# Kernel optimization log

Hardware: AMD Instinct MI355X
Metric: run time of the kernel (lower is better)

Reference implementation:

```python
import jax, jax.numpy as jnp
import numpy as np
from jax import lax

B, L = 8, 128
V, P = 30000, 50
EMB, POS = 300, 30
H = 256            # rnn_hidden per direction
H2 = 2 * H         # BiLSTM output dim
NBIO, NLAB = 9, 10
ROUNDS = 2
IN = EMB + POS
NEG = -100000000000.0


def setup_inputs() -> dict:
    key = jax.random.key(0)
    ks = jax.random.split(key, 25)
    tokens = jax.random.randint(ks[0], (B, L), 1, V)
    pos = jax.random.randint(ks[1], (B, L), 1, P)
    lens = jax.random.randint(ks[2], (B,), L // 2, L + 1)
    mask_s = (jnp.arange(L)[None, :] < lens[:, None]).astype(jnp.float32)

    def g(k, shape, s=0.05):
        return jax.random.normal(k, shape, dtype=jnp.float32) * s

    return dict(
        tokens=tokens, pos=pos, mask_s=mask_s,
        emb=g(ks[3], (V, EMB), 0.5), pos_emb=g(ks[4], (P, POS), 0.5),
        Wih_f=g(ks[5], (4 * H, IN)), Whh_f=g(ks[6], (4 * H, H)), b_f=g(ks[7], (4 * H,)),
        Wih_b=g(ks[8], (4 * H, IN)), Whh_b=g(ks[9], (4 * H, H)), b_b=g(ks[10], (4 * H,)),
        Wg_ih=g(ks[11], (3 * H2, NBIO)), Wg_hh=g(ks[12], (3 * H2, H2)),
        bg_ih=g(ks[13], (3 * H2,)), bg_hh=g(ks[14], (3 * H2,)),
        Wr_ih=g(ks[15], (3 * H2, NLAB)), Wr_hh=g(ks[16], (3 * H2, H2)),
        br_ih=g(ks[17], (3 * H2,)), br_hh=g(ks[18], (3 * H2,)),
        W_Lr=g(ks[19], (H2, 2 * H2)), b_Lr=g(ks[20], (H2,)),
        W_Cr=g(ks[21], (NLAB, H2)), b_Cr=g(ks[22], (NLAB,)),
        W_Cg=g(ks[23], (NBIO, H2)), b_Cg=g(ks[24], (NBIO,)),
    )


def lstm_dir(x, m, Wih, Whh, b, reverse):
    # x: [B,L,IN], m: [B,L]. Masked updates emulate pack_padded_sequence
    # (state held at padded steps; padded outputs zeroed by caller).
    Bn = x.shape[0]
    h0 = jnp.zeros((Bn, H), x.dtype)
    c0 = jnp.zeros((Bn, H), x.dtype)

    def step(carry, inp):
        h, c = carry
        xt, mt = inp  # [B,IN], [B,1]
        gates = xt @ Wih.T + h @ Whh.T + b
        i, f, g, o = jnp.split(gates, 4, axis=-1)
        i = jax.nn.sigmoid(i); f = jax.nn.sigmoid(f)
        g = jnp.tanh(g); o = jax.nn.sigmoid(o)
        c_new = f * c + i * g
        h_new = o * jnp.tanh(c_new)
        h = mt * h_new + (1.0 - mt) * h
        c = mt * c_new + (1.0 - mt) * c
        return (h, c), h

    xs = (jnp.swapaxes(x, 0, 1), m.T[:, :, None])
    _, hs = lax.scan(step, (h0, c0), xs, reverse=reverse)
    return jnp.swapaxes(hs, 0, 1)  # [B,L,H]


def gru_cell(x, h, Wih, Whh, bih, bhh):
    gi = x @ Wih.T + bih
    gh = h @ Whh.T + bhh
    ir, iz, inn = jnp.split(gi, 3, axis=-1)
    hr, hz, hn = jnp.split(gh, 3, axis=-1)
    r = jax.nn.sigmoid(ir + hr)
    z = jax.nn.sigmoid(iz + hz)
    n = jnp.tanh(inn + r * hn)
    return (1.0 - z) * n + z * h


def pair_scores(Hr, W_Lr, b_Lr, W_Cr, b_Cr):
    # Lr([e1;e2]) split: e12 @ W_Lr.T = e1 @ W1.T + e2 @ W2.T (avoids 4H concat)
    W1, W2 = W_Lr[:, :H2], W_Lr[:, H2:]
    a = jnp.einsum('blh,oh->blo', Hr, W1)  # [B,L,H2]
    b2 = jnp.einsum('blh,oh->blo', Hr, W2)
    e = jax.nn.relu(a[:, :, None, :] + b2[:, None, :, :] + b_Lr)  # [B,L,L,H2]
    return jax.nn.sigmoid(jnp.einsum('bsth,kh->bstk', e, W_Cr) + b_Cr)  # [B,L,L,NLAB]


def reference(tokens, pos, mask_s, emb, pos_emb,
              Wih_f, Whh_f, b_f, Wih_b, Whh_b, b_b,
              Wg_ih, Wg_hh, bg_ih, bg_hh,
              Wr_ih, Wr_hh, br_ih, br_hh,
              W_Lr, b_Lr, W_Cr, b_Cr, W_Cg, b_Cg):
    x = jnp.concatenate([emb[tokens], pos_emb[pos]], axis=2)  # [B,L,IN]
    hf = lstm_dir(x, mask_s, Wih_f, Whh_f, b_f, reverse=False)
    hb = lstm_dir(x, mask_s, Wih_b, Whh_b, b_b, reverse=True)
    Henc = jnp.concatenate([hf, hb], axis=2) * mask_s[:, :, None]  # [B,L,H2]

    m2 = mask_s[:, :, None] * mask_s[:, None, :]  # [B,L,L] pair mask
    m3 = m2[:, :, :, None]                        # [B,L,L,1]

    Hc, Hg, Hr = Henc, Henc, Henc
    for _ in range(ROUNDS):
        prob_Cg = jax.nn.softmax(Hg @ W_Cg.T + b_Cg, axis=2)        # [B,L,NBIO]
        prob_Cr = pair_scores(Hr, W_Lr, b_Lr, W_Cr, b_Cr)            # [B,L,L,NLAB]
        prob_Cr = jnp.where(m3 > 0, prob_Cr, NEG)
        prob_Cr = prob_Cr.max(axis=2)                                # [B,L,NLAB]
        hflat = Hc.reshape(-1, H2)
        Hg = gru_cell(prob_Cg.reshape(-1, NBIO), hflat, Wg_ih, Wg_hh, bg_ih, bg_hh).reshape(Hc.shape)
        Hr = gru_cell(prob_Cr.reshape(-1, NLAB), hflat, Wr_ih, Wr_hh, br_ih, br_hh).reshape(Hc.shape)
        Hc = Hc + Hr + Hg

    logits_Cg = jax.nn.log_softmax(Hg @ W_Cg.T + b_Cg, axis=2) * mask_s[:, :, None]
    logits_Cr = pair_scores(Hr, W_Lr, b_Lr, W_Cr, b_Cr) * m3
    return logits_Cg, logits_Cr
```

## Files before the change

### kernel.cpp

```cpp
#include <hip/hip_runtime.h>
#include <hip/hip_bf16.h>
#include <stdint.h>

#define DEVI __device__ __forceinline__

static constexpr int Bn = 8, Ln = 128;
static constexpr int EMBc = 300, POSc = 30, INc = 330;
static constexpr int KPAD = 384;
static constexpr int Hc = 256, H2c = 512, G4 = 1024, G3 = 1536;
static constexpr int G2 = 2048;
static constexpr int GHW = 3072;
static constexpr int NBIOc = 9, NLABc = 10;
static constexpr float NEGc = -100000000000.0f;

typedef __attribute__((ext_vector_type(8))) short bf16x8;
typedef __attribute__((ext_vector_type(4))) float f32x4;

DEVI float sigf(float x) { return 1.0f / (1.0f + __expf(-x)); }

DEVI unsigned short b16rne(float f) {
    union { float f; unsigned u; } v; v.f = f;
    unsigned u = v.u;
    return (unsigned short)((u + 0x7FFFu + ((u >> 16) & 1u)) >> 16);
}

__global__ void k_prep0(const int* __restrict__ tok, const int* __restrict__ pos,
                        const float* __restrict__ emb, const float* __restrict__ pemb,
                        const float* __restrict__ WihF, const float* __restrict__ WihB,
                        const float* __restrict__ bF, const float* __restrict__ bB,
                        ushort* __restrict__ x, ushort* __restrict__ WihFB,
                        float* __restrict__ biasFB) {
    int i = blockIdx.x * 256 + threadIdx.x;
    const int N0 = Bn * Ln * KPAD;
    const int N1 = N0 + G2 * KPAD;
    if (i < N0) {
        int bl = i / KPAD, c = i - bl * KPAD;
        float v = 0.f;
        if (c < EMBc) v = emb[tok[bl] * EMBc + c];
        else if (c < INc) v = pemb[pos[bl] * POSc + (c - EMBc)];
        x[i] = b16rne(v);
    } else if (i < N1) {
        int w = i - N0;
        int r = w / KPAD, c = w - r * KPAD;
        float v = 0.f;
        if (c < INc) v = (r < G4) ? WihF[(size_t)r * INc + c] : WihB[(size_t)(r - G4) * INc + c];
        WihFB[w] = b16rne(v);
    } else if (i < N1 + G2) {
        int j = i - N1;
        biasFB[j] = (j < G4) ? bF[j] : bB[j - G4];
    }
}

__global__ __launch_bounds__(256) void k_gemm_bf(
    const ushort* __restrict__ A, const ushort* __restrict__ B,
    const float* __restrict__ bias, float* __restrict__ C, int M, int N, int K) {
    __shared__ __align__(16) ushort As[64][72];
    __shared__ __align__(16) ushort Bs[64][72];
    int tid = threadIdx.x;
    int lane = tid & 63, wv = tid >> 6;
    int m0 = blockIdx.y * 64, n0 = blockIdx.x * 64;
    int mw = (wv >> 1) * 32, nw = (wv & 1) * 32;
    int lr16 = lane & 15, g4 = lane >> 4;
    f32x4 acc[2][2] = {};
    for (int k0 = 0; k0 < K; k0 += 64) {
#pragma unroll
        for (int it = 0; it < 2; it++) {
            int idx = tid + it * 256;
            int r = idx >> 3, ch = idx & 7;
            uint4 av = *(const uint4*)(A + (size_t)(m0 + r) * K + k0 + ch * 8);
            *(uint4*)(&As[r][ch * 8]) = av;
            uint4 bv2 = *(const uint4*)(B + (size_t)(n0 + r) * K + k0 + ch * 8);
            *(uint4*)(&Bs[r][ch * 8]) = bv2;
        }
        __syncthreads();
#pragma unroll
        for (int ks = 0; ks < 2; ks++) {
            bf16x8 af[2], bfr[2];
#pragma unroll
            for (int i = 0; i < 2; i++) {
                af[i]  = *(const bf16x8*)(&As[mw + i * 16 + lr16][ks * 32 + g4 * 8]);
                bfr[i] = *(const bf16x8*)(&Bs[nw + i * 16 + lr16][ks * 32 + g4 * 8]);
            }
#pragma unroll
            for (int i = 0; i < 2; i++)
#pragma unroll
                for (int j = 0; j < 2; j++)
                    acc[i][j] = __builtin_amdgcn_mfma_f32_16x16x32_bf16(af[i], bfr[j], acc[i][j], 0, 0, 0);
        }
        __syncthreads();
    }
#pragma unroll
    for (int i = 0; i < 2; i++)
#pragma unroll
        for (int j = 0; j < 2; j++)
#pragma unroll
            for (int r2 = 0; r2 < 4; r2++) {
                int mm = m0 + mw + i * 16 + g4 * 4 + r2;
                int nn = n0 + nw + j * 16 + lr16;
                C[(size_t)mm * N + nn] = acc[i][j][r2] + (bias ? bias[nn] : 0.f);
            }
}

__global__ __launch_bounds__(512) void k_lstm_mfma(
    const float* __restrict__ Xpre,
    const float* __restrict__ WhhF, const float* __restrict__ WhhB,
    const float* __restrict__ mask, float* __restrict__ Henc,
    ushort* __restrict__ HencB, unsigned long long* __restrict__ hG,
    const float* __restrict__ Wg_hh, const float* __restrict__ Wr_hh,
    const float* __restrict__ W_Lr, const float* __restrict__ bg_hh,
    const float* __restrict__ br_hh,
    ushort* __restrict__ WhhGR, ushort* __restrict__ WLrAB, float* __restrict__ biasGR) {
    const int blk = blockIdx.x;
    const int tid = threadIdx.x;

    if (blk >= 8) {
        const int stride = 32 * 512;
        int pid = (blk - 8) * 512 + tid;
        for (int idx = pid; idx < GHW * H2c; idx += stride) {
            int r = idx >> 9, c = idx & 511;
            float v = (r < G3) ? Wg_hh[(size_t)r * H2c + c] : Wr_hh[(size_t)(r - G3) * H2c + c];
            WhhGR[idx] = b16rne(v);
        }
        for (int idx = pid; idx < G4 * H2c; idx += stride) {
            int r = idx >> 9, c = idx & 511;
            float v = (r < H2c) ? W_Lr[(size_t)r * (2 * H2c) + c]
                                : W_Lr[(size_t)(r - H2c) * (2 * H2c) + H2c + c];
            WLrAB[idx] = b16rne(v);
        }
        for (int idx = pid; idx < GHW; idx += stride)
            biasGR[idx] = (idx < G3) ? bg_hh[idx] : br_hh[idx - G3];
        return;
    }

    const int d = blk >> 2, q = blk & 3;
    const float* Whh = d ? WhhB : WhhF;
    const int lane = tid & 63, wv = tid >> 6;
    const int lr16 = lane & 15, g4 = lane >> 4;

    __shared__ __align__(16) uint32_t hlds[2][8 * 136];
    __shared__ float Glds[256][9];

    bf16x8 aw[16];
#pragma unroll
    for (int jt2 = 0; jt2 < 2; jt2++) {
        int jt = wv * 2 + jt2;
        int lr = jt * 16 + lr16;
        int g = lr >> 6, jj = lr & 63;
        int R = g * 256 + q * 64 + jj;
        const float* wr = Whh + (size_t)R * 256;
#pragma unroll
        for (int kt = 0; kt < 8; kt++) {
            int k0 = kt * 32 + g4 * 8;
            float4 f0 = *(const float4*)(wr + k0);
            float4 f1 = *(const float4*)(wr + k0 + 4);
            bf16x8 a;
            a[0] = (short)b16rne(f0.x); a[1] = (short)b16rne(f0.y);
            a[2] = (short)b16rne(f0.z); a[3] = (short)b16rne(f0.w);
            a[4] = (short)b16rne(f1.x); a[5] = (short)b16rne(f1.y);
            a[6] = (short)b16rne(f1.z); a[7] = (short)b16rne(f1.w);
            aw[jt2 * 8 + kt] = a;
        }
    }

    const int jj_t = tid & 63, b_t = tid >> 6;
    float hval = 0.f, cval = 0.f;
    const int bcol = lane & 15;
    const int bb = lane & 7;
    const int u1 = tid + 512;

    for (int s = 0; s < Ln; s++) {
        const int t = d ? (Ln - 1 - s) : s;

        const float* xrow = Xpre + ((size_t)(b_t * Ln + t)) * G2 + d * G4 + q * 64 + jj_t;
        float xg0 = xrow[0], xg1 = xrow[256], xg2 = xrow[512], xg3 = xrow[768];
        float mval = mask[b_t * Ln + t];

        const unsigned long long* slot = hG + ((size_t)(s & 1) * 2 + d) * 1024;
        unsigned long long ea, eb;
        do {
            ea = __hip_atomic_load(slot + tid, __ATOMIC_RELAXED, __HIP_MEMORY_SCOPE_AGENT);
            eb = __hip_atomic_load(slot + u1,  __ATOMIC_RELAXED, __HIP_MEMORY_SCOPE_AGENT);
        } while ((unsigned)(ea >> 32) != (unsigned)s || (unsigned)(eb >> 32) != (unsigned)s);
        uint32_t* hb = hlds[s & 1];
        hb[(tid >> 7) * 136 + (tid & 127)] = (uint32_t)ea;
        hb[(u1 >> 7) * 136 + (u1 & 127)]  = (uint32_t)eb;
        __syncthreads();

        bf16x8 bv[8];
#pragma unroll
        for (int kt = 0; kt < 8; kt++)
            bv[kt] = *(const bf16x8*)(&hb[bb * 136 + kt * 16 + g4 * 4]);

        f32x4 acc0 = {0.f, 0.f, 0.f, 0.f}, acc1 = {0.f, 0.f, 0.f, 0.f};
#pragma unroll
        for (int kt = 0; kt < 8; kt++) {
            acc0 = __builtin_amdgcn_mfma_f32_16x16x32_bf16(aw[kt], bv[kt], acc0, 0, 0, 0);
            acc1 = __builtin_amdgcn_mfma_f32_16x16x32_bf16(aw[8 + kt], bv[kt], acc1, 0, 0, 0);
        }

        if (bcol < 8) {
            int lrb0 = (wv * 2 + 0) * 16 + g4 * 4;
            int lrb1 = (wv * 2 + 1) * 16 + g4 * 4;
#pragma unroll
            for (int r2 = 0; r2 < 4; r2++) Glds[lrb0 + r2][bcol] = acc0[r2];
#pragma unroll
            for (int r2 = 0; r2 < 4; r2++) Glds[lrb1 + r2][bcol] = acc1[r2];
        }
        __syncthreads();

        float iv = sigf(xg0 + Glds[jj_t][b_t]);
        float fv = sigf(xg1 + Glds[64 + jj_t][b_t]);
        float gv = tanhf(xg2 + Glds[128 + jj_t][b_t]);
        float ov = sigf(xg3 + Glds[192 + jj_t][b_t]);
        float cn = fv * cval + iv * gv;
        float hn = ov * tanhf(cn);
        float hv = mval * hn + (1.f - mval) * hval;
        cval = mval * cn + (1.f - mval) * cval;
        hval = hv;

        int hbits = (int)b16rne(hv);
        int pbits = __shfl_xor(hbits, 1);
        if ((jj_t & 1) == 0) {
            uint32_t dataw = ((uint32_t)hbits & 0xFFFFu) | ((uint32_t)pbits << 16);
            unsigned long long word = ((unsigned long long)(unsigned)(s + 1) << 32) | dataw;
            __hip_atomic_store(hG + ((size_t)((s + 1) & 1) * 2 + d) * 1024 +
                                   b_t * 128 + q * 32 + (jj_t >> 1),
                               word, __ATOMIC_RELAXED, __HIP_MEMORY_SCOPE_AGENT);
        }
        float ho = hv * mval;
        size_t hidx = ((size_t)(b_t * Ln + t)) * H2c + d * Hc + q * 64 + jj_t;
        Henc[hidx] = ho;
        HencB[hidx] = b16rne(ho);
    }
}

__global__ __launch_bounds__(256) void k_proj9(
    const float* __restrict__ H, const float* __restrict__ W,
    const float* __restrict__ b, float* __restrict__ out) {
    int lane = threadIdx.x & 63, wv = threadIdx.x >> 6;
    int row = blockIdx.x * 4 + wv;
    const float4* h4 = (const float4*)(H + (size_t)row * H2c + lane * 8);
    float4 h0 = h4[0], h1 = h4[1];
    float acc[NBIOc];
#pragma unroll
    for (int k = 0; k < NBIOc; k++) {
        const float4* w4 = (const float4*)(W + (size_t)k * H2c + lane * 8);
        float4 w0 = w4[0], w1 = w4[1];
        acc[k] = h0.x * w0.x + h0.y * w0.y + h0.z * w0.z + h0.w * w0.w +
                 h1.x * w1.x + h1.y * w1.y + h1.z * w1.z + h1.w * w1.w;
    }
#pragma unroll
    for (int off = 32; off >= 1; off >>= 1)
#pragma unroll
        for (int k = 0; k < NBIOc; k++) acc[k] += __shfl_down(acc[k], off);
    if (lane == 0) {
#pragma unroll
        for (int k = 0; k < NBIOc; k++) out[(size_t)row * NBIOc + k] = acc[k] + b[k];
    }
}

__global__ void k_logsoftmax9(const float* __restrict__ lg, const float* __restrict__ mask,
                              float* __restrict__ outp) {
    int r = blockIdx.x * 256 + threadIdx.x;
    if (r >= Bn * Ln) return;
    float v[NBIOc], mx = -3.4e38f;
#pragma unroll
    for (int k = 0; k < NBIOc; k++) { v[k] = lg[r * NBIOc + k]; mx = fmaxf(mx, v[k]); }
    float s = 0.f;
#pragma unroll
    for (int k = 0; k < NBIOc; k++) s += __expf(v[k] - mx);
    float lse = mx + __logf(s);
    float m = mask[r];
#pragma unroll
    for (int k = 0; k < NBIOc; k++) outp[r * NBIOc + k] = (v[k] - lse) * m;
}

__global__ __launch_bounds__(128) void k_pairmax(
    const float* __restrict__ Cp, const float* __restrict__ bL,
    const float* __restrict__ WCr, const float* __restrict__ bCr,
    const float* __restrict__ mask, float* __restrict__ probCr) {
    int bs = blockIdx.x;
    int b = bs >> 7;
    __shared__ __align__(16) float As[H2c];
    __shared__ __align__(16) float Ws[NLABc][H2c];
    __shared__ float red[NLABc][128];
    int tid = threadIdx.x;
    for (int i = tid; i < H2c; i += 128) As[i] = Cp[(size_t)bs * G4 + i] + bL[i];
    for (int i = tid; i < NLABc * H2c; i += 128) Ws[i / H2c][i % H2c] = WCr[i];
    __syncthreads();
    int t = tid;
    float m3 = mask[bs] * mask[b * Ln + t];
    float outv[NLABc];
    if (m3 > 0.f) {
        float4 acc[NLABc];
#pragma unroll
        for (int k = 0; k < NLABc; k++) acc[k] = make_float4(0.f, 0.f, 0.f, 0.f);
        const float4* B4 = (const float4*)(Cp + (size_t)(b * Ln + t) * G4 + H2c);
        const float4* A4 = (const float4*)As;
        for (int qq = 0; qq < H2c / 4; qq++) {
            float4 a = A4[qq], bb = B4[qq];
            float4 e;
            e.x = fmaxf(a.x + bb.x, 0.f);
            e.y = fmaxf(a.y + bb.y, 0.f);
            e.z = fmaxf(a.z + bb.z, 0.f);
            e.w = fmaxf(a.w + bb.w, 0.f);
#pragma unroll
            for (int k = 0; k < NLABc; k++) {
                float4 w = *(const float4*)(&Ws[k][qq * 4]);
                acc[k].x += e.x * w.x; acc[k].y += e.y * w.y;
                acc[k].z += e.z * w.z; acc[k].w += e.w * w.w;
            }
        }
#pragma unroll
        for (int k = 0; k < NLABc; k++)
            outv[k] = sigf(acc[k].x + acc[k].y + acc[k].z + acc[k].w + bCr[k]);
    } else {
#pragma unroll
        for (int k = 0; k < NLABc; k++) outv[k] = NEGc;
    }
#pragma unroll
    for (int k = 0; k < NLABc; k++) red[k][tid] = outv[k];
    __syncthreads();
    for (int off = 64; off >= 1; off >>= 1) {
        if (tid < off) {
#pragma unroll
            for (int k = 0; k < NLABc; k++) red[k][tid] = fmaxf(red[k][tid], red[k][tid + off]);
        }
        __syncthreads();
    }
    if (tid < NLABc) probCr[bs * NLABc + tid] = red[tid][0];
}

__global__ __launch_bounds__(128) void k_pairfull(
    const float* __restrict__ Cp, const float* __restrict__ bL,
    const float* __restrict__ WCr, const float* __restrict__ bCr,
    const float* __restrict__ mask, float* __restrict__ outCr) {
    int bs = blockIdx.x;
    int b = bs >> 7;
    __shared__ __align__(16) float As[H2c];
    __shared__ __align__(16) float Ws[NLABc][H2c];
    int tid = threadIdx.x;
    for (int i = tid; i < H2c; i += 128) As[i] = Cp[(size_t)bs * G4 + i] + bL[i];
    for (int i = tid; i < NLABc * H2c; i += 128) Ws[i / H2c][i % H2c] = WCr[i];
    __syncthreads();
    int t = tid;
    float m3 = mask[bs] * mask[b * Ln + t];
    float outv[NLABc];
    if (m3 > 0.f) {
        float4 acc[NLABc];
#pragma unroll
        for (int k = 0; k < NLABc; k++) acc[k] = make_float4(0.f, 0.f, 0.f, 0.f);
        const float4* B4 = (const float4*)(Cp + (size_t)(b * Ln + t) * G4 + H2c);
        const float4* A4 = (const float4*)As;
        for (int qq = 0; qq < H2c / 4; qq++) {
            float4 a = A4[qq], bb = B4[qq];
            float4 e;
            e.x = fmaxf(a.x + bb.x, 0.f);
            e.y = fmaxf(a.y + bb.y, 0.f);
            e.z = fmaxf(a.z + bb.z, 0.f);
            e.w = fmaxf(a.w + bb.w, 0.f);
#pragma unroll
            for (int k = 0; k < NLABc; k++) {
                float4 w = *(const float4*)(&Ws[k][qq * 4]);
                acc[k].x += e.x * w.x; acc[k].y += e.y * w.y;
                acc[k].z += e.z * w.z; acc[k].w += e.w * w.w;
            }
        }
#pragma unroll
        for (int k = 0; k < NLABc; k++)
            outv[k] = sigf(acc[k].x + acc[k].y + acc[k].z + acc[k].w + bCr[k]);
    } else {
#pragma unroll
        for (int k = 0; k < NLABc; k++) outv[k] = 0.f;
    }
    size_t base = ((size_t)bs * Ln + t) * NLABc;
#pragma unroll
    for (int k = 0; k < NLABc; k++) outCr[base + k] = outv[k];
}

__global__ void k_gru2(const float* __restrict__ gh ,
                       const float* __restrict__ cg, const float* __restrict__ pCr,
                       const float* __restrict__ Wg_ih, const float* __restrict__ bg_ih,
                       const float* __restrict__ Wr_ih, const float* __restrict__ br_ih,
                       const float* __restrict__ hprev,
                       float* __restrict__ Hg_out, float* __restrict__ Hcb_out,
                       ushort* __restrict__ Hrb_out, ushort* __restrict__ Hcbb_out) {
    int i = blockIdx.x * 256 + threadIdx.x;
    if (i >= Bn * Ln * H2c) return;
    int m = i >> 9, j = i & 511;

    float v[NBIOc], mx = -3.4e38f;
#pragma unroll
    for (int k = 0; k < NBIOc; k++) { v[k] = cg[m * NBIOc + k]; mx = fmaxf(mx, v[k]); }
    float ssum = 0.f;
#pragma unroll
    for (int k = 0; k < NBIOc; k++) { v[k] = __expf(v[k] - mx); ssum += v[k]; }
    float inv = 1.f / ssum;

    float gr = bg_ih[j], gz = bg_ih[H2c + j], gn = bg_ih[2 * H2c + j];
#pragma unroll
    for (int k = 0; k < NBIOc; k++) {
        float pv = v[k] * inv;
        gr += Wg_ih[(size_t)j * NBIOc + k] * pv;
        gz += Wg_ih[(size_t)(H2c + j) * NBIOc + k] * pv;
        gn += Wg_ih[(size_t)(2 * H2c + j) * NBIOc + k] * pv;
    }
    const float* g1 = gh + (size_t)m * GHW;
    float hp = hprev[i];
    float r1 = sigf(gr + g1[j]);
    float z1 = sigf(gz + g1[H2c + j]);
    float n1 = tanhf(gn + r1 * g1[2 * H2c + j]);
    float hg = (1.f - z1) * n1 + z1 * hp;

    float rr = br_ih[j], rz = br_ih[H2c + j], rn = br_ih[2 * H2c + j];
    const float* p = pCr + (size_t)m * NLABc;
#pragma unroll
    for (int k = 0; k < NLABc; k++) {
        float pv = p[k];
        rr += Wr_ih[(size_t)j * NLABc + k] * pv;
        rz += Wr_ih[(size_t)(H2c + j) * NLABc + k] * pv;
        rn += Wr_ih[(size_t)(2 * H2c + j) * NLABc + k] * pv;
    }
    const float* g2 = g1 + G3;
    float r2 = sigf(rr + g2[j]);
    float z2 = sigf(rz + g2[H2c + j]);
    float n2 = tanhf(rn + r2 * g2[2 * H2c + j]);
    float hr = (1.f - z2) * n2 + z2 * hp;

    float hc = hp + hr + hg;
    Hg_out[i] = hg;
    Hcb_out[i] = hc;
    Hrb_out[i] = b16rne(hr);
    Hcbb_out[i] = b16rne(hc);
}

extern "C" void kernel_launch(void* const* d_in, const int* in_sizes, int n_in,
                              void* d_out, int out_size, void* d_ws, size_t ws_size,
                              hipStream_t stream) {
    const int*   tok   = (const int*)d_in[0];
    const int*   pos   = (const int*)d_in[1];
    const float* mask  = (const float*)d_in[2];
    const float* emb   = (const float*)d_in[3];
    const float* pemb  = (const float*)d_in[4];
    const float* WihF  = (const float*)d_in[5];
    const float* WhhF  = (const float*)d_in[6];
    const float* bF    = (const float*)d_in[7];
    const float* WihB  = (const float*)d_in[8];
    const float* WhhB  = (const float*)d_in[9];
    const float* bB    = (const float*)d_in[10];
    const float* Wg_ih = (const float*)d_in[11];
    const float* Wg_hh = (const float*)d_in[12];
    const float* bg_ih = (const float*)d_in[13];
    const float* bg_hh = (const float*)d_in[14];
    const float* Wr_ih = (const float*)d_in[15];
    const float* Wr_hh = (const float*)d_in[16];
    const float* br_ih = (const float*)d_in[17];
    const float* br_hh = (const float*)d_in[18];
    const float* W_Lr  = (const float*)d_in[19];
    const float* b_Lr  = (const float*)d_in[20];
    const float* W_Cr  = (const float*)d_in[21];
    const float* b_Cr  = (const float*)d_in[22];
    const float* W_Cg  = (const float*)d_in[23];
    const float* b_Cg  = (const float*)d_in[24];

    float* outp = (float*)d_out;
    float* ws = (float*)d_ws;

    unsigned long long* hG = (unsigned long long*)ws;
    size_t off = 8192;
    auto alloc = [&](size_t n) { off = (off + 3) & ~(size_t)3; float* p = ws + off; off += n; return p; };
    auto allocU = [&](size_t n_us) { off = (off + 3) & ~(size_t)3; ushort* p = (ushort*)(ws + off); off += (n_us + 1) / 2; return p; };

    float* R1 = alloc((size_t)G4 * GHW);
    float* Xpre  = R1;
    float* pairC = R1;
    float* gh    = R1;
    ushort* WihFB_bf = (ushort*)(R1 + (size_t)G4 * G2);
    ushort* x_bf     = (ushort*)(R1 + (size_t)G4 * G2 + 393216);
    float*  biasFB   = R1 + (size_t)G4 * G2 + 393216 + 196608;

    ushort* WhhGR_bf = allocU((size_t)GHW * H2c);
    ushort* WLrAB_bf = allocU((size_t)G4 * H2c);
    float*  biasGR   = alloc(GHW);
    float*  Henc     = alloc((size_t)Bn * Ln * H2c);
    ushort* Henc_bf  = allocU((size_t)Bn * Ln * H2c);
    float*  Hg       = alloc((size_t)Bn * Ln * H2c);
    float*  Hcb      = alloc((size_t)Bn * Ln * H2c);
    ushort* Hr_bf    = allocU((size_t)Bn * Ln * H2c);
    ushort* Hcb_bf   = allocU((size_t)Bn * Ln * H2c);
    float*  cg       = alloc((size_t)Bn * Ln * NBIOc);
    float*  pCr      = alloc((size_t)Bn * Ln * NLABc);
    (void)ws_size; (void)in_sizes; (void)n_in; (void)out_size;

    auto gemm_bf = [&](const ushort* A, const ushort* B, const float* bias,
                       float* C, int M, int N, int K) {
        dim3 g(N / 64, M / 64);
        k_gemm_bf<<<g, 256, 0, stream>>>(A, B, bias, C, M, N, K);
    };

    hipMemsetAsync(hG, 0, 8192 * sizeof(float), stream);

    {
        int total = Bn * Ln * KPAD + G2 * KPAD + G2;
        k_prep0<<<(total + 255) / 256, 256, 0, stream>>>(
            tok, pos, emb, pemb, WihF, WihB, bF, bB, x_bf, WihFB_bf, biasFB);
    }

    gemm_bf(x_bf, WihFB_bf, biasFB, Xpre, Bn * Ln, G2, KPAD);

    k_lstm_mfma<<<40, 512, 0, stream>>>(Xpre, WhhF, WhhB, mask, Henc, Henc_bf, hG,
                                        Wg_hh, Wr_hh, W_Lr, bg_hh, br_hh,
                                        WhhGR_bf, WLrAB_bf, biasGR);

    const float*  Hgs    = Henc;
    const ushort* Hrs_bf = Henc_bf;
    const float*  Hcs    = Henc;
    const ushort* Hcs_bf = Henc_bf;
    for (int r = 0; r < 2; r++) {
        k_proj9<<<Bn * Ln / 4, 256, 0, stream>>>(Hgs, W_Cg, b_Cg, cg);

        gemm_bf(Hrs_bf, WLrAB_bf, nullptr, pairC, Bn * Ln, G4, H2c);
        k_pairmax<<<Bn * Ln, 128, 0, stream>>>(pairC, b_Lr, W_Cr, b_Cr, mask, pCr);

        gemm_bf(Hcs_bf, WhhGR_bf, biasGR, gh, Bn * Ln, GHW, H2c);
        k_gru2<<<(Bn * Ln * H2c + 255) / 256, 256, 0, stream>>>(
            gh, cg, pCr, Wg_ih, bg_ih, Wr_ih, br_ih, Hcs, Hg, Hcb, Hr_bf, Hcb_bf);

        Hgs = Hg; Hrs_bf = Hr_bf; Hcs = Hcb; Hcs_bf = Hcb_bf;
    }

    k_proj9<<<Bn * Ln / 4, 256, 0, stream>>>(Hgs, W_Cg, b_Cg, cg);
    k_logsoftmax9<<<4, 256, 0, stream>>>(cg, mask, outp);

    gemm_bf(Hrs_bf, WLrAB_bf, nullptr, pairC, Bn * Ln, G4, H2c);
    k_pairfull<<<Bn * Ln, 128, 0, stream>>>(pairC, b_Lr, W_Cr, b_Cr, mask,
                                            outp + Bn * Ln * NBIOc);
}
```

Measured before the change: 483.2 us.

## Fuse independent GEMMs and projections into combined launches; drop LDS gate exchange in LSTM

```diff
diff --git a/kernel.cpp b/kernel.cpp
--- a/kernel.cpp
+++ b/kernel.cpp
@@ -51,14 +51,12 @@
     }
 }
 
-__global__ __launch_bounds__(256) void k_gemm_bf(
-    const ushort* __restrict__ A, const ushort* __restrict__ B,
-    const float* __restrict__ bias, float* __restrict__ C, int M, int N, int K) {
-    __shared__ __align__(16) ushort As[64][72];
-    __shared__ __align__(16) ushort Bs[64][72];
+DEVI void gemm_tile(const ushort* __restrict__ A, const ushort* __restrict__ B,
+                    const float* __restrict__ bias, float* __restrict__ C,
+                    int N, int K, int m0, int n0,
+                    ushort (*As)[72], ushort (*Bs)[72]) {
     int tid = threadIdx.x;
     int lane = tid & 63, wv = tid >> 6;
-    int m0 = blockIdx.y * 64, n0 = blockIdx.x * 64;
     int mw = (wv >> 1) * 32, nw = (wv & 1) * 32;
     int lr16 = lane & 15, g4 = lane >> 4;
     f32x4 acc[2][2] = {};
@@ -101,52 +99,57 @@
             }
 }
 
-__global__ __launch_bounds__(512) void k_lstm_mfma(
-    const float* __restrict__ Xpre,
-    const float* __restrict__ WhhF, const float* __restrict__ WhhB,
-    const float* __restrict__ mask, float* __restrict__ Henc,
-    ushort* __restrict__ HencB, unsigned long long* __restrict__ hG,
+__global__ __launch_bounds__(256) void k_xproj(
+    const ushort* __restrict__ x_bf, const ushort* __restrict__ WihFB,
+    const float* __restrict__ biasFB, float* __restrict__ Xpre,
     const float* __restrict__ Wg_hh, const float* __restrict__ Wr_hh,
     const float* __restrict__ W_Lr, const float* __restrict__ bg_hh,
     const float* __restrict__ br_hh,
     ushort* __restrict__ WhhGR, ushort* __restrict__ WLrAB, float* __restrict__ biasGR) {
+    int bid = blockIdx.x;
+    __shared__ __align__(16) ushort As[64][72];
+    __shared__ __align__(16) ushort Bs[64][72];
+    if (bid < 512) {
+        int nt = bid & 31, mt = bid >> 5;
+        gemm_tile(x_bf, WihFB, biasFB, Xpre, G2, KPAD, mt * 64, nt * 64, As, Bs);
+        return;
+    }
+    const int stride = 32 * 256;
+    int pid = (bid - 512) * 256 + threadIdx.x;
+    for (int idx = pid; idx < GHW * H2c; idx += stride) {
+        int r = idx >> 9, c = idx & 511;
+        float v = (r < G3) ? Wg_hh[(size_t)r * H2c + c] : Wr_hh[(size_t)(r - G3) * H2c + c];
+        WhhGR[idx] = b16rne(v);
+    }
+    for (int idx = pid; idx < G4 * H2c; idx += stride) {
+        int r = idx >> 9, c = idx & 511;
+        float v = (r < H2c) ? W_Lr[(size_t)r * (2 * H2c) + c]
+                            : W_Lr[(size_t)(r - H2c) * (2 * H2c) + H2c + c];
+        WLrAB[idx] = b16rne(v);
+    }
+    for (int idx = pid; idx < GHW; idx += stride)
+        biasGR[idx] = (idx < G3) ? bg_hh[idx] : br_hh[idx - G3];
+}
+
+__global__ __launch_bounds__(512) void k_lstm_mfma(
+    const float* __restrict__ Xpre, const float* __restrict__ WhhF,
+    const float* __restrict__ WhhB, const float* __restrict__ mask,
+    float* __restrict__ Henc, ushort* __restrict__ HencB,
+    unsigned long long* __restrict__ hG) {
     const int blk = blockIdx.x;
-    const int tid = threadIdx.x;
-
-    if (blk >= 8) {
-        const int stride = 32 * 512;
-        int pid = (blk - 8) * 512 + tid;
-        for (int idx = pid; idx < GHW * H2c; idx += stride) {
-            int r = idx >> 9, c = idx & 511;
-            float v = (r < G3) ? Wg_hh[(size_t)r * H2c + c] : Wr_hh[(size_t)(r - G3) * H2c + c];
-            WhhGR[idx] = b16rne(v);
-        }
-        for (int idx = pid; idx < G4 * H2c; idx += stride) {
-            int r = idx >> 9, c = idx & 511;
-            float v = (r < H2c) ? W_Lr[(size_t)r * (2 * H2c) + c]
-                                : W_Lr[(size_t)(r - H2c) * (2 * H2c) + H2c + c];
-            WLrAB[idx] = b16rne(v);
-        }
-        for (int idx = pid; idx < GHW; idx += stride)
-            biasGR[idx] = (idx < G3) ? bg_hh[idx] : br_hh[idx - G3];
-        return;
-    }
-
     const int d = blk >> 2, q = blk & 3;
     const float* Whh = d ? WhhB : WhhF;
+    const int tid = threadIdx.x;
     const int lane = tid & 63, wv = tid >> 6;
     const int lr16 = lane & 15, g4 = lane >> 4;
 
     __shared__ __align__(16) uint32_t hlds[2][8 * 136];
-    __shared__ float Glds[256][9];
 
     bf16x8 aw[16];
 #pragma unroll
     for (int jt2 = 0; jt2 < 2; jt2++) {
-        int jt = wv * 2 + jt2;
-        int lr = jt * 16 + lr16;
-        int g = lr >> 6, jj = lr & 63;
-        int R = g * 256 + q * 64 + jj;
+        int L = (wv * 2 + jt2) * 16 + lr16;
+        int R = (L & 3) * 256 + q * 64 + (L >> 2);
         const float* wr = Whh + (size_t)R * 256;
 #pragma unroll
         for (int kt = 0; kt < 8; kt++) {
@@ -162,18 +165,22 @@
         }
     }
 
-    const int jj_t = tid & 63, b_t = tid >> 6;
-    float hval = 0.f, cval = 0.f;
     const int bcol = lane & 15;
+    const bool act = (bcol < 8);
     const int bb = lane & 7;
     const int u1 = tid + 512;
+    float hv0 = 0.f, cv0 = 0.f, hv1 = 0.f, cv1 = 0.f;
 
     for (int s = 0; s < Ln; s++) {
         const int t = d ? (Ln - 1 - s) : s;
 
-        const float* xrow = Xpre + ((size_t)(b_t * Ln + t)) * G2 + d * G4 + q * 64 + jj_t;
-        float xg0 = xrow[0], xg1 = xrow[256], xg2 = xrow[512], xg3 = xrow[768];
-        float mval = mask[b_t * Ln + t];
+        float xg0[4], xg1[4], mval = 0.f;
+        if (act) {
+            const float* xb = Xpre + ((size_t)(bcol * Ln + t)) * G2 + d * G4 + q * 64 + 8 * wv + g4;
+#pragma unroll
+            for (int g = 0; g < 4; g++) { xg0[g] = xb[g * 256]; xg1[g] = xb[g * 256 + 4]; }
+            mval = mask[bcol * Ln + t];
+        }
 
         const unsigned long long* slot = hG + ((size_t)(s & 1) * 2 + d) * 1024;
         unsigned long long ea, eb;
@@ -198,81 +205,96 @@
             acc1 = __builtin_amdgcn_mfma_f32_16x16x32_bf16(aw[8 + kt], bv[kt], acc1, 0, 0, 0);
         }
 
-        if (bcol < 8) {
-            int lrb0 = (wv * 2 + 0) * 16 + g4 * 4;
-            int lrb1 = (wv * 2 + 1) * 16 + g4 * 4;
-#pragma unroll
-            for (int r2 = 0; r2 < 4; r2++) Glds[lrb0 + r2][bcol] = acc0[r2];
-#pragma unroll
-            for (int r2 = 0; r2 < 4; r2++) Glds[lrb1 + r2][bcol] = acc1[r2];
-        }
-        __syncthreads();
-
-        float iv = sigf(xg0 + Glds[jj_t][b_t]);
-        float fv = sigf(xg1 + Glds[64 + jj_t][b_t]);
-        float gv = tanhf(xg2 + Glds[128 + jj_t][b_t]);
-        float ov = sigf(xg3 + Glds[192 + jj_t][b_t]);
-        float cn = fv * cval + iv * gv;
-        float hn = ov * tanhf(cn);
-        float hv = mval * hn + (1.f - mval) * hval;
-        cval = mval * cn + (1.f - mval) * cval;
-        hval = hv;
-
-        int hbits = (int)b16rne(hv);
-        int pbits = __shfl_xor(hbits, 1);
-        if ((jj_t & 1) == 0) {
-            uint32_t dataw = ((uint32_t)hbits & 0xFFFFu) | ((uint32_t)pbits << 16);
+        int h0bits = 0, h1bits = 0;
+        if (act) {
+            float iv = sigf(xg0[0] + acc0[0]);
+            float fv = sigf(xg0[1] + acc0[1]);
+            float gv = tanhf(xg0[2] + acc0[2]);
+            float ov = sigf(xg0[3] + acc0[3]);
+            float cn = fv * cv0 + iv * gv;
+            float hn = ov * tanhf(cn);
+            float h = mval * hn + (1.f - mval) * hv0;
+            cv0 = mval * cn + (1.f - mval) * cv0;
+            hv0 = h;
+
+            iv = sigf(xg1[0] + acc1[0]);
+            fv = sigf(xg1[1] + acc1[1]);
+            gv = tanhf(xg1[2] + acc1[2]);
+            ov = sigf(xg1[3] + acc1[3]);
+            cn = fv * cv1 + iv * gv;
+            hn = ov * tanhf(cn);
+            h = mval * hn + (1.f - mval) * hv1;
+            cv1 = mval * cn + (1.f - mval) * cv1;
+            hv1 = h;
+
+            h0bits = (int)b16rne(hv0);
+            h1bits = (int)b16rne(hv1);
+        }
+        int e0 = __shfl_xor(h0bits, 16);
+        int e1 = __shfl_xor(h1bits, 16);
+        if (act) {
+            uint32_t dataw; int pc;
+            if ((g4 & 1) == 0) {
+                dataw = ((uint32_t)h0bits & 0xFFFFu) | ((uint32_t)e0 << 16);
+                pc = g4 >> 1;
+            } else {
+                dataw = ((uint32_t)e1 & 0xFFFFu) | ((uint32_t)h1bits << 16);
+                pc = 2 + (g4 >> 1);
+            }
             unsigned long long word = ((unsigned long long)(unsigned)(s + 1) << 32) | dataw;
             __hip_atomic_store(hG + ((size_t)((s + 1) & 1) * 2 + d) * 1024 +
-                                   b_t * 128 + q * 32 + (jj_t >> 1),
+                                   bcol * 128 + q * 32 + wv * 4 + pc,
                                word, __ATOMIC_RELAXED, __HIP_MEMORY_SCOPE_AGENT);
-        }
-        float ho = hv * mval;
-        size_t hidx = ((size_t)(b_t * Ln + t)) * H2c + d * Hc + q * 64 + jj_t;
-        Henc[hidx] = ho;
-        HencB[hidx] = b16rne(ho);
-    }
-}
-
-__global__ __launch_bounds__(256) void k_proj9(
-    const float* __restrict__ H, const float* __restrict__ W,
-    const float* __restrict__ b, float* __restrict__ out) {
-    int lane = threadIdx.x & 63, wv = threadIdx.x >> 6;
-    int row = blockIdx.x * 4 + wv;
-    const float4* h4 = (const float4*)(H + (size_t)row * H2c + lane * 8);
-    float4 h0 = h4[0], h1 = h4[1];
-    float acc[NBIOc];
-#pragma unroll
-    for (int k = 0; k < NBIOc; k++) {
-        const float4* w4 = (const float4*)(W + (size_t)k * H2c + lane * 8);
-        float4 w0 = w4[0], w1 = w4[1];
-        acc[k] = h0.x * w0.x + h0.y * w0.y + h0.z * w0.z + h0.w * w0.w +
-                 h1.x * w1.x + h1.y * w1.y + h1.z * w1.z + h1.w * w1.w;
-    }
-#pragma unroll
-    for (int off = 32; off >= 1; off >>= 1)
-#pragma unroll
-        for (int k = 0; k < NBIOc; k++) acc[k] += __shfl_down(acc[k], off);
-    if (lane == 0) {
-#pragma unroll
-        for (int k = 0; k < NBIOc; k++) out[(size_t)row * NBIOc + k] = acc[k] + b[k];
-    }
-}
-
-__global__ void k_logsoftmax9(const float* __restrict__ lg, const float* __restrict__ mask,
-                              float* __restrict__ outp) {
-    int r = blockIdx.x * 256 + threadIdx.x;
-    if (r >= Bn * Ln) return;
-    float v[NBIOc], mx = -3.4e38f;
-#pragma unroll
-    for (int k = 0; k < NBIOc; k++) { v[k] = lg[r * NBIOc + k]; mx = fmaxf(mx, v[k]); }
-    float s = 0.f;
-#pragma unroll
-    for (int k = 0; k < NBIOc; k++) s += __expf(v[k] - mx);
-    float lse = mx + __logf(s);
-    float m = mask[r];
-#pragma unroll
-    for (int k = 0; k < NBIOc; k++) outp[r * NBIOc + k] = (v[k] - lse) * m;
+
+            float ho0 = hv0 * mval, ho1 = hv1 * mval;
+            size_t base = ((size_t)(bcol * Ln + t)) * H2c + d * Hc + q * 64 + 8 * wv + g4;
+            Henc[base] = ho0;     Henc[base + 4] = ho1;
+            HencB[base] = b16rne(ho0); HencB[base + 4] = b16rne(ho1);
+        }
+    }
+}
+
+__global__ __launch_bounds__(256) void k_mega(
+    int nGh,
+    const ushort* __restrict__ Agh, const ushort* __restrict__ Bgh,
+    const float* __restrict__ biasGh, float* __restrict__ Cgh,
+    const ushort* __restrict__ Apc, const ushort* __restrict__ Bpc,
+    float* __restrict__ Cpc,
+    const float* __restrict__ Hp9, const float* __restrict__ W9,
+    const float* __restrict__ b9, float* __restrict__ out9) {
+    int bid = blockIdx.x;
+    __shared__ __align__(16) ushort As[64][72];
+    __shared__ __align__(16) ushort Bs[64][72];
+    if (bid < nGh) {
+        int nt = bid % 48, mt = bid / 48;
+        gemm_tile(Agh, Bgh, biasGh, Cgh, GHW, H2c, mt * 64, nt * 64, As, Bs);
+    } else if (bid < nGh + 256) {
+        int b2 = bid - nGh;
+        int nt = b2 & 15, mt = b2 >> 4;
+        gemm_tile(Apc, Bpc, nullptr, Cpc, G4, H2c, mt * 64, nt * 64, As, Bs);
+    } else {
+        int b3 = bid - nGh - 256;
+        int lane = threadIdx.x & 63, wvv = threadIdx.x >> 6;
+        int row = b3 * 4 + wvv;
+        const float4* h4 = (const float4*)(Hp9 + (size_t)row * H2c + lane * 8);
+        float4 h0 = h4[0], h1 = h4[1];
+        float acc[NBIOc];
+#pragma unroll
+        for (int k = 0; k < NBIOc; k++) {
+            const float4* w4 = (const float4*)(W9 + (size_t)k * H2c + lane * 8);
+            float4 w0 = w4[0], w1 = w4[1];
+            acc[k] = h0.x * w0.x + h0.y * w0.y + h0.z * w0.z + h0.w * w0.w +
+                     h1.x * w1.x + h1.y * w1.y + h1.z * w1.z + h1.w * w1.w;
+        }
+#pragma unroll
+        for (int off = 32; off >= 1; off >>= 1)
+#pragma unroll
+            for (int k = 0; k < NBIOc; k++) acc[k] += __shfl_down(acc[k], off);
+        if (lane == 0) {
+#pragma unroll
+            for (int k = 0; k < NBIOc; k++) out9[(size_t)row * NBIOc + k] = acc[k] + b9[k];
+        }
+    }
 }
 
 __global__ __launch_bounds__(128) void k_pairmax(
@@ -331,15 +353,87 @@
     if (tid < NLABc) probCr[bs * NLABc + tid] = red[tid][0];
 }
 
-__global__ __launch_bounds__(128) void k_pairfull(
+__global__ void k_gru2(const float* __restrict__ gh,
+                       const float* __restrict__ cg, const float* __restrict__ pCr,
+                       const float* __restrict__ Wg_ih, const float* __restrict__ bg_ih,
+                       const float* __restrict__ Wr_ih, const float* __restrict__ br_ih,
+                       const float* __restrict__ hprev,
+                       float* __restrict__ Hg_out, float* __restrict__ Hcb_out,
+                       ushort* __restrict__ Hrb_out, ushort* __restrict__ Hcbb_out) {
+    int i = blockIdx.x * 256 + threadIdx.x;
+    if (i >= Bn * Ln * H2c) return;
+    int m = i >> 9, j = i & 511;
+
+    float v[NBIOc], mx = -3.4e38f;
+#pragma unroll
+    for (int k = 0; k < NBIOc; k++) { v[k] = cg[m * NBIOc + k]; mx = fmaxf(mx, v[k]); }
+    float ssum = 0.f;
+#pragma unroll
+    for (int k = 0; k < NBIOc; k++) { v[k] = __expf(v[k] - mx); ssum += v[k]; }
+    float inv = 1.f / ssum;
+
+    float gr = bg_ih[j], gz = bg_ih[H2c + j], gn = bg_ih[2 * H2c + j];
+#pragma unroll
+    for (int k = 0; k < NBIOc; k++) {
+        float pv = v[k] * inv;
+        gr += Wg_ih[(size_t)j * NBIOc + k] * pv;
+        gz += Wg_ih[(size_t)(H2c + j) * NBIOc + k] * pv;
+        gn += Wg_ih[(size_t)(2 * H2c + j) * NBIOc + k] * pv;
+    }
+    const float* g1 = gh + (size_t)m * GHW;
+    float hp = hprev[i];
+    float r1 = sigf(gr + g1[j]);
+    float z1 = sigf(gz + g1[H2c + j]);
+    float n1 = tanhf(gn + r1 * g1[2 * H2c + j]);
+    float hg = (1.f - z1) * n1 + z1 * hp;
+
+    float rr = br_ih[j], rz = br_ih[H2c + j], rn = br_ih[2 * H2c + j];
+    const float* p = pCr + (size_t)m * NLABc;
+#pragma unroll
+    for (int k = 0; k < NLABc; k++) {
+        float pv = p[k];
+        rr += Wr_ih[(size_t)j * NLABc + k] * pv;
+        rz += Wr_ih[(size_t)(H2c + j) * NLABc + k] * pv;
+        rn += Wr_ih[(size_t)(2 * H2c + j) * NLABc + k] * pv;
+    }
+    const float* g2 = g1 + G3;
+    float r2 = sigf(rr + g2[j]);
+    float z2 = sigf(rz + g2[H2c + j]);
+    float n2 = tanhf(rn + r2 * g2[2 * H2c + j]);
+    float hr = (1.f - z2) * n2 + z2 * hp;
+
+    float hc = hp + hr + hg;
+    Hg_out[i] = hg;
+    Hcb_out[i] = hc;
+    Hrb_out[i] = b16rne(hr);
+    Hcbb_out[i] = b16rne(hc);
+}
+
+__global__ __launch_bounds__(128) void k_final_out(
     const float* __restrict__ Cp, const float* __restrict__ bL,
     const float* __restrict__ WCr, const float* __restrict__ bCr,
-    const float* __restrict__ mask, float* __restrict__ outCr) {
-    int bs = blockIdx.x;
+    const float* __restrict__ mask, const float* __restrict__ cg,
+    float* __restrict__ outp) {
+    int bid = blockIdx.x;
+    int tid = threadIdx.x;
+    if (bid >= Bn * Ln) {
+        int r = (bid - Bn * Ln) * 128 + tid;
+        float v[NBIOc], mx = -3.4e38f;
+#pragma unroll
+        for (int k = 0; k < NBIOc; k++) { v[k] = cg[r * NBIOc + k]; mx = fmaxf(mx, v[k]); }
+        float s = 0.f;
+#pragma unroll
+        for (int k = 0; k < NBIOc; k++) s += __expf(v[k] - mx);
+        float lse = mx + __logf(s);
+        float m = mask[r];
+#pragma unroll
+        for (int k = 0; k < NBIOc; k++) outp[r * NBIOc + k] = (v[k] - lse) * m;
+        return;
+    }
+    int bs = bid;
     int b = bs >> 7;
     __shared__ __align__(16) float As[H2c];
     __shared__ __align__(16) float Ws[NLABc][H2c];
-    int tid = threadIdx.x;
     for (int i = tid; i < H2c; i += 128) As[i] = Cp[(size_t)bs * G4 + i] + bL[i];
     for (int i = tid; i < NLABc * H2c; i += 128) Ws[i / H2c][i % H2c] = WCr[i];
     __syncthreads();
@@ -373,65 +467,9 @@
 #pragma unroll
         for (int k = 0; k < NLABc; k++) outv[k] = 0.f;
     }
-    size_t base = ((size_t)bs * Ln + t) * NLABc;
-#pragma unroll
-    for (int k = 0; k < NLABc; k++) outCr[base + k] = outv[k];
-}
-
-__global__ void k_gru2(const float* __restrict__ gh ,
-                       const float* __restrict__ cg, const float* __restrict__ pCr,
-                       const float* __restrict__ Wg_ih, const float* __restrict__ bg_ih,
-                       const float* __restrict__ Wr_ih, const float* __restrict__ br_ih,
-                       const float* __restrict__ hprev,
-                       float* __restrict__ Hg_out, float* __restrict__ Hcb_out,
-                       ushort* __restrict__ Hrb_out, ushort* __restrict__ Hcbb_out) {
-    int i = blockIdx.x * 256 + threadIdx.x;
-    if (i >= Bn * Ln * H2c) return;
-    int m = i >> 9, j = i & 511;
-
-    float v[NBIOc], mx = -3.4e38f;
-#pragma unroll
-    for (int k = 0; k < NBIOc; k++) { v[k] = cg[m * NBIOc + k]; mx = fmaxf(mx, v[k]); }
-    float ssum = 0.f;
-#pragma unroll
-    for (int k = 0; k < NBIOc; k++) { v[k] = __expf(v[k] - mx); ssum += v[k]; }
-    float inv = 1.f / ssum;
-
-    float gr = bg_ih[j], gz = bg_ih[H2c + j], gn = bg_ih[2 * H2c + j];
-#pragma unroll
-    for (int k = 0; k < NBIOc; k++) {
-        float pv = v[k] * inv;
-        gr += Wg_ih[(size_t)j * NBIOc + k] * pv;
-        gz += Wg_ih[(size_t)(H2c + j) * NBIOc + k] * pv;
-        gn += Wg_ih[(size_t)(2 * H2c + j) * NBIOc + k] * pv;
-    }
-    const float* g1 = gh + (size_t)m * GHW;
-    float hp = hprev[i];
-    float r1 = sigf(gr + g1[j]);
-    float z1 = sigf(gz + g1[H2c + j]);
-    float n1 = tanhf(gn + r1 * g1[2 * H2c + j]);
-    float hg = (1.f - z1) * n1 + z1 * hp;
-
-    float rr = br_ih[j], rz = br_ih[H2c + j], rn = br_ih[2 * H2c + j];
-    const float* p = pCr + (size_t)m * NLABc;
-#pragma unroll
-    for (int k = 0; k < NLABc; k++) {
-        float pv = p[k];
-        rr += Wr_ih[(size_t)j * NLABc + k] * pv;
-        rz += Wr_ih[(size_t)(H2c + j) * NLABc + k] * pv;
-        rn += Wr_ih[(size_t)(2 * H2c + j) * NLABc + k] * pv;
-    }
-    const float* g2 = g1 + G3;
-    float r2 = sigf(rr + g2[j]);
-    float z2 = sigf(rz + g2[H2c + j]);
-    float n2 = tanhf(rn + r2 * g2[2 * H2c + j]);
-    float hr = (1.f - z2) * n2 + z2 * hp;
-
-    float hc = hp + hr + hg;
-    Hg_out[i] = hg;
-    Hcb_out[i] = hc;
-    Hrb_out[i] = b16rne(hr);
-    Hcbb_out[i] = b16rne(hc);
+    size_t base = (size_t)(Bn * Ln * NBIOc) + ((size_t)bs * Ln + t) * NLABc;
+#pragma unroll
+    for (int k = 0; k < NLABc; k++) outp[base + k] = outv[k];
 }
 
 extern "C" void kernel_launch(void* const* d_in, const int* in_sizes, int n_in,
@@ -472,13 +510,13 @@
     auto allocU = [&](size_t n_us) { off = (off + 3) & ~(size_t)3; ushort* p = (ushort*)(ws + off); off += (n_us + 1) / 2; return p; };
 
     float* R1 = alloc((size_t)G4 * GHW);
-    float* Xpre  = R1;
-    float* pairC = R1;
-    float* gh    = R1;
+    float* Xpre = R1;
+    float* gh   = R1;
     ushort* WihFB_bf = (ushort*)(R1 + (size_t)G4 * G2);
     ushort* x_bf     = (ushort*)(R1 + (size_t)G4 * G2 + 393216);
     float*  biasFB   = R1 + (size_t)G4 * G2 + 393216 + 196608;
 
+    float*  pairC    = alloc((size_t)G4 * G4);
     ushort* WhhGR_bf = allocU((size_t)GHW * H2c);
     ushort* WLrAB_bf = allocU((size_t)G4 * H2c);
     float*  biasGR   = alloc(GHW);
@@ -492,12 +530,6 @@
     float*  pCr      = alloc((size_t)Bn * Ln * NLABc);
     (void)ws_size; (void)in_sizes; (void)n_in; (void)out_size;
 
-    auto gemm_bf = [&](const ushort* A, const ushort* B, const float* bias,
-                       float* C, int M, int N, int K) {
-        dim3 g(N / 64, M / 64);
-        k_gemm_bf<<<g, 256, 0, stream>>>(A, B, bias, C, M, N, K);
-    };
-
     hipMemsetAsync(hG, 0, 8192 * sizeof(float), stream);
 
     {
@@ -506,33 +538,30 @@
             tok, pos, emb, pemb, WihF, WihB, bF, bB, x_bf, WihFB_bf, biasFB);
     }
 
-    gemm_bf(x_bf, WihFB_bf, biasFB, Xpre, Bn * Ln, G2, KPAD);
-
-    k_lstm_mfma<<<40, 512, 0, stream>>>(Xpre, WhhF, WhhB, mask, Henc, Henc_bf, hG,
-                                        Wg_hh, Wr_hh, W_Lr, bg_hh, br_hh,
-                                        WhhGR_bf, WLrAB_bf, biasGR);
+    k_xproj<<<544, 256, 0, stream>>>(x_bf, WihFB_bf, biasFB, Xpre,
+                                     Wg_hh, Wr_hh, W_Lr, bg_hh, br_hh,
+                                     WhhGR_bf, WLrAB_bf, biasGR);
+
+    k_lstm_mfma<<<8, 512, 0, stream>>>(Xpre, WhhF, WhhB, mask, Henc, Henc_bf, hG);
 
     const float*  Hgs    = Henc;
     const ushort* Hrs_bf = Henc_bf;
     const float*  Hcs    = Henc;
     const ushort* Hcs_bf = Henc_bf;
     for (int r = 0; r < 2; r++) {
-        k_proj9<<<Bn * Ln / 4, 256, 0, stream>>>(Hgs, W_Cg, b_Cg, cg);
-
-        gemm_bf(Hrs_bf, WLrAB_bf, nullptr, pairC, Bn * Ln, G4, H2c);
+        k_mega<<<768 + 512, 256, 0, stream>>>(768,
+            Hcs_bf, WhhGR_bf, biasGR, gh,
+            Hrs_bf, WLrAB_bf, pairC,
+            Hgs, W_Cg, b_Cg, cg);
         k_pairmax<<<Bn * Ln, 128, 0, stream>>>(pairC, b_Lr, W_Cr, b_Cr, mask, pCr);
-
-        gemm_bf(Hcs_bf, WhhGR_bf, biasGR, gh, Bn * Ln, GHW, H2c);
         k_gru2<<<(Bn * Ln * H2c + 255) / 256, 256, 0, stream>>>(
             gh, cg, pCr, Wg_ih, bg_ih, Wr_ih, br_ih, Hcs, Hg, Hcb, Hr_bf, Hcb_bf);
-
         Hgs = Hg; Hrs_bf = Hr_bf; Hcs = Hcb; Hcs_bf = Hcb_bf;
     }
 
-    k_proj9<<<Bn * Ln / 4, 256, 0, stream>>>(Hgs, W_Cg, b_Cg, cg);
-    k_logsoftmax9<<<4, 256, 0, stream>>>(cg, mask, outp);
-
-    gemm_bf(Hrs_bf, WLrAB_bf, nullptr, pairC, Bn * Ln, G4, H2c);
-    k_pairfull<<<Bn * Ln, 128, 0, stream>>>(pairC, b_Lr, W_Cr, b_Cr, mask,
-                                            outp + Bn * Ln * NBIOc);
-}
+    k_mega<<<512, 256, 0, stream>>>(0,
+        nullptr, nullptr, nullptr, nullptr,
+        Hrs_bf, WLrAB_bf, pairC,
+        Hgs, W_Cg, b_Cg, cg);
+    k_final_out<<<Bn * Ln + 8, 128, 0, stream>>>(pairC, b_Lr, W_Cr, b_Cr, mask, cg, outp);
+}
```

Result: slower. 674.3 us (+39.6%).
